# Kernel optimization log

Hardware: AMD Instinct MI355X
Metric: run time of the kernel (lower is better)

Reference implementation:

```python
import jax, jax.numpy as jnp
import numpy as np
from jax import lax

D_H = 1024
RES_DIMS = (512, 256)
LAYERS = 2
T = 8192
ALPHA = 0.1  # reservoir leak rate


def setup_inputs() -> dict:
    key = jax.random.key(0)
    ks = jax.random.split(key, 8)
    s_h = 1.0 / np.sqrt(D_H)
    s_r1 = 1.0 / np.sqrt(RES_DIMS[0])
    s_r2 = 1.0 / np.sqrt(RES_DIMS[1])
    return {
        "x_seq": jax.random.normal(ks[0], (T, D_H), jnp.float32),
        "Wx": jax.random.normal(ks[1], (LAYERS, D_H, D_H), jnp.float32) * s_h,
        "Wh": jax.random.normal(ks[2], (LAYERS, D_H, D_H), jnp.float32) * s_h,
        "b": jnp.zeros((LAYERS, D_H), jnp.float32),
        "V1": jax.random.normal(ks[3], (LAYERS, D_H, RES_DIMS[0]), jnp.float32) * s_r1,
        "U1": jax.random.normal(ks[4], (LAYERS, RES_DIMS[0], D_H), jnp.float32) * s_h,
        "V2": jax.random.normal(ks[5], (LAYERS, D_H, RES_DIMS[1]), jnp.float32) * s_r2,
        "U2": jax.random.normal(ks[6], (LAYERS, RES_DIMS[1], D_H), jnp.float32) * s_h,
    }


def reference(x_seq, Wx, Wh, b, V1, U1, V2, U2):
    # CRSDBlock: stacked recurrent layers, each a time scan with hidden h and
    # two leaky reservoirs. h' = tanh(Wx x + Wh h + V1 r1 + V2 r2 + b);
    # r_i' = (1-a) r_i + a tanh(U_i h').
    d_h = Wx.shape[-1]
    d_r1, d_r2 = U1.shape[1], U2.shape[1]
    dt = x_seq.dtype
    for l in range(Wx.shape[0]):
        wx, wh, bb = Wx[l], Wh[l], b[l]
        v1, u1, v2, u2 = V1[l], U1[l], V2[l], U2[l]

        def step(carry, x_t):
            h, r1, r2 = carry
            h = jnp.tanh(x_t @ wx.T + h @ wh.T + r1 @ v1.T + r2 @ v2.T + bb)
            r1 = (1.0 - ALPHA) * r1 + ALPHA * jnp.tanh(h @ u1.T)
            r2 = (1.0 - ALPHA) * r2 + ALPHA * jnp.tanh(h @ u2.T)
            return (h, r1, r2), h

        init = (jnp.zeros((d_h,), dt), jnp.zeros((d_r1,), dt), jnp.zeros((d_r2,), dt))
        _, x_seq = lax.scan(step, init, x_seq)
    return x_seq
```

## Files before the change

### kernel.cpp

```cpp
#include <hip/hip_runtime.h>

#define D_HH   1024
#define DR1    512
#define DR2    256
#define RTOT   (DR1 + DR2)
#define TSTEPS 8192

#define NB     64
#define BS     512
#define HA     (D_HH / NB)
#define QA     (RTOT / NB)
#define NROWB  (HA + QA)
#define RING   64
#define RMASK  (RING - 1)
#define NREP   4

typedef __attribute__((ext_vector_type(2))) unsigned long long ull2;

__device__ __forceinline__ float dot4f(float4 a, float4 b) {
    return fmaf(a.x, b.x, fmaf(a.y, b.y, fmaf(a.z, b.z, a.w * b.w)));
}

__device__ __forceinline__ ull2 ld16(const unsigned long long* p) {
    ull2 v;
    asm volatile("global_load_dwordx4 %0, %1, off sc0 sc1\n\ts_waitcnt vmcnt(0)"
                 : "=&v"(v) : "v"(p) : "memory");
    return v;
}
__device__ __forceinline__ void ld16x2(const unsigned long long* p0,
                                       const unsigned long long* p1,
                                       ull2& a, ull2& b) {
    asm volatile("global_load_dwordx4 %0, %2, off sc0 sc1\n\t"
                 "global_load_dwordx4 %1, %3, off sc0 sc1\n\t"
                 "s_waitcnt vmcnt(0)"
                 : "=&v"(a), "=&v"(b) : "v"(p0), "v"(p1) : "memory");
}
__device__ __forceinline__ unsigned long long ld8(const unsigned long long* p) {
    unsigned long long v;
    asm volatile("global_load_dwordx2 %0, %1, off sc0 sc1\n\ts_waitcnt vmcnt(0)"
                 : "=&v"(v) : "v"(p) : "memory");
    return v;
}
__device__ __forceinline__ void st16(unsigned long long* p,
                                     unsigned long long lo, unsigned long long hi) {
    ull2 pv; pv[0] = lo; pv[1] = hi;
    asm volatile("global_store_dwordx4 %0, %1, off sc0 sc1"
                 :: "v"(p), "v"(pv) : "memory");
}
__device__ __forceinline__ void st8(unsigned long long* p, int tag, unsigned pay) {
    unsigned long long pv = ((unsigned long long)(unsigned)tag << 32) | pay;
    asm volatile("global_store_dwordx2 %0, %1, off sc0 sc1"
                 :: "v"(p), "v"(pv) : "memory");
}
__device__ __forceinline__ unsigned long long mktag(int tag, float v) {
    return ((unsigned long long)(unsigned)tag << 32) | __float_as_uint(v);
}

__global__ __launch_bounds__(BS, 2) void crsd_fused(
    const float* __restrict__ x,
    const float* __restrict__ Wx,
    const float* __restrict__ Wh,
    const float* __restrict__ bias,
    const float* __restrict__ V1,
    const float* __restrict__ U1,
    const float* __restrict__ V2,
    const float* __restrict__ U2,
    float* __restrict__ out,
    unsigned long long* ring,
    unsigned long long* h1rep,
    unsigned long long* h2rep,
    unsigned long long* r1rep,
    unsigned long long* r2rep,
    unsigned long long* prog)
{
    const int gid = blockIdx.x;
    const int lay = gid >> 6;
    const int g   = gid & (NB - 1);
    const int tid = threadIdx.x;

    const float* wxp = Wx + (size_t)lay * D_HH * D_HH;
    const float* whp = Wh + (size_t)lay * D_HH * D_HH;
    const float* v1p = V1 + (size_t)lay * D_HH * DR1;
    const float* v2p = V2 + (size_t)lay * D_HH * DR2;
    const float* u1p = U1 + (size_t)lay * DR1 * D_HH;
    const float* u2p = U2 + (size_t)lay * DR2 * D_HH;
    const float* bp  = bias + (size_t)lay * D_HH;
    unsigned long long* rrep = lay ? r2rep : r1rep;
    unsigned long long* hrep = lay ? h2rep : h1rep;
    const int rep = g & (NREP - 1);

    __shared__ __align__(16) float r_s[RTOT];
    __shared__ __align__(16) float h_s[D_HH];
    __shared__ __align__(16) float x_s[D_HH];
    __shared__ float zw[HA];

    const int rA = tid >> 5;
    const int p  = tid & 31;
    const int iA = g * HA + rA;
    float4 wa[6];
    {
        const float4* v1r = (const float4*)(v1p + (size_t)iA * DR1);
#pragma unroll
        for (int k = 0; k < 4; ++k) wa[k] = v1r[p + 32 * k];
        const float4* v2r = (const float4*)(v2p + (size_t)iA * DR2);
#pragma unroll
        for (int k = 0; k < 2; ++k) wa[4 + k] = v2r[p + 32 * k];
    }

    const int rB = tid >> 4;
    const int q  = tid & 15;
    const bool isZ = (rB < HA);
    const bool isQ = (rB >= HA) && (rB < NROWB);
    int jG = 0;
    float bi = 0.f;
    const float* brow = whp;
    const float* xrow = whp;
    if (isZ) {
        brow = whp + (size_t)(g * HA + rB) * D_HH;
        xrow = wxp + (size_t)(g * HA + rB) * D_HH;
        bi   = bp[g * HA + rB];
    } else if (isQ) {
        jG = g * QA + (rB - HA);
        brow = (jG < DR1) ? (u1p + (size_t)jG * D_HH)
                          : (u2p + (size_t)(jG - DR1) * D_HH);
    }
    float4 wb[16], wxr[16];
    {
        const float4* br = (const float4*)brow;
        const float4* xr = (const float4*)xrow;
#pragma unroll
        for (int k = 0; k < 16; ++k) { wb[k] = br[q + 16 * k]; wxr[k] = xr[q + 16 * k]; }
    }

    float rloc0 = 0.f, rloc1 = 0.f;
    int   l2c   = 0;

    if (lay == 0) {
        float2 xv = *(const float2*)&x[2 * tid];
        *(float2*)&x_s[2 * tid] = xv;
    } else {
        const unsigned long long* px0 = &ring[2 * tid];
        for (;;) {
            ull2 v = ld16(px0);
            if ((int)(v[0] >> 32) >= 1 && (int)(v[1] >> 32) >= 1) {
                *(float2*)&x_s[2 * tid] =
                    make_float2(__uint_as_float((unsigned)v[0]),
                                __uint_as_float((unsigned)v[1]));
                break;
            }
            __builtin_amdgcn_s_sleep(1);
        }
    }
    __syncthreads();
    if (isZ) {
        const float4* x4 = (const float4*)x_s;
        float acc = 0.f;
#pragma unroll
        for (int k = 0; k < 16; ++k) acc += dot4f(wxr[k], x4[q + 16 * k]);
#pragma unroll
        for (int m = 8; m >= 1; m >>= 1) acc += __shfl_xor(acc, m);
        if (q == 0) zw[rB] = bi + acc;
    }

    for (int t = 0; t < TSTEPS; ++t) {
        if (lay == 0 && tid == 0 && t - 60 > l2c) {
            for (;;) {
                unsigned long long v = ld8(prog);
                if ((int)(v >> 32) >= t - 60) { l2c = (int)(v >> 32); break; }
                __builtin_amdgcn_s_sleep(1);
            }
        }

        if (tid < RTOT / 2) {
            const unsigned long long* pr = &rrep[rep * RTOT + 2 * tid];
            for (;;) {
                ull2 v = ld16(pr);
                if ((int)(v[0] >> 32) >= t && (int)(v[1] >> 32) >= t) {
                    *(float2*)&r_s[2 * tid] =
                        make_float2(__uint_as_float((unsigned)v[0]),
                                    __uint_as_float((unsigned)v[1]));
                    break;
                }
                __builtin_amdgcn_s_sleep(1);
            }
        }
        __syncthreads();

        {
            const float4* r1v = (const float4*)r_s;
            const float4* r2v = (const float4*)(r_s + DR1);
            float acc = dot4f(wa[0], r1v[p]);
            acc += dot4f(wa[1], r1v[p + 32]);
            acc += dot4f(wa[2], r1v[p + 64]);
            acc += dot4f(wa[3], r1v[p + 96]);
            acc += dot4f(wa[4], r2v[p]);
            acc += dot4f(wa[5], r2v[p + 32]);
#pragma unroll
            for (int m = 16; m >= 1; m >>= 1) acc += __shfl_xor(acc, m);
            float hv  = tanhf(zw[rA] + acc);
            float hvp = __shfl_xor(hv, 32);
            if ((tid & 63) == 0) {
                unsigned long long e0 = mktag(t + 1, hv);
                unsigned long long e1 = mktag(t + 1, hvp);
#pragma unroll
                for (int k = 0; k < NREP; ++k)
                    st16(&hrep[k * D_HH + iA], e0, e1);
                if (lay == 0) {
                    st16(&ring[(size_t)(t & RMASK) * D_HH + iA], e0, e1);
                } else {
                    *(float2*)&out[(size_t)t * D_HH + iA] = make_float2(hv, hvp);
                    if (iA == 0) st8(prog, t + 1, 0u);
                }
                *(float2*)&h_s[iA] = make_float2(hv, hvp);
            }
        }

        if (lay == 0) {
            const int ti = (t + 1 < TSTEPS) ? t + 1 : TSTEPS - 1;
            float2 xv = *(const float2*)&x[(size_t)ti * D_HH + 2 * tid];
            *(float2*)&x_s[2 * tid] = xv;
        }

        {
            bool dh = ((tid >> 3) == g);
            const unsigned long long* ph = &hrep[rep * D_HH + 2 * tid];
            if (lay == 0) {
                if (!dh) {
                    for (;;) {
                        ull2 v = ld16(ph);
                        if ((int)(v[0] >> 32) >= t + 1 && (int)(v[1] >> 32) >= t + 1) {
                            *(float2*)&h_s[2 * tid] =
                                make_float2(__uint_as_float((unsigned)v[0]),
                                            __uint_as_float((unsigned)v[1]));
                            break;
                        }
                        __builtin_amdgcn_s_sleep(1);
                    }
                }
            } else {
                const bool needx = (t + 1 < TSTEPS);
                bool dx = !needx;
                const unsigned long long* px =
                    &ring[(size_t)((t + 1) & RMASK) * D_HH + 2 * tid];
                while (!(dh && dx)) {
                    ull2 a, b;
                    ld16x2(ph, px, a, b);
                    if (!dh && (int)(a[0] >> 32) >= t + 1 && (int)(a[1] >> 32) >= t + 1) {
                        *(float2*)&h_s[2 * tid] =
                            make_float2(__uint_as_float((unsigned)a[0]),
                                        __uint_as_float((unsigned)a[1]));
                        dh = true;
                    }
                    if (!dx && (int)(b[0] >> 32) >= t + 2 && (int)(b[1] >> 32) >= t + 2) {
                        *(float2*)&x_s[2 * tid] =
                            make_float2(__uint_as_float((unsigned)b[0]),
                                        __uint_as_float((unsigned)b[1]));
                        dx = true;
                    }
                    if (!(dh && dx)) __builtin_amdgcn_s_sleep(1);
                }
            }
        }
        __syncthreads();

        if (rB < NROWB) {
            const float4* h4 = (const float4*)h_s;
            float acc = 0.f;
#pragma unroll
            for (int k = 0; k < 16; ++k) acc += dot4f(wb[k], h4[q + 16 * k]);
            if (isZ) {
                const float4* x4 = (const float4*)x_s;
#pragma unroll
                for (int k = 0; k < 16; ++k) acc += dot4f(wxr[k], x4[q + 16 * k]);
            }
#pragma unroll
            for (int m = 8; m >= 1; m >>= 1) acc += __shfl_xor(acc, m);
            if (isZ) {
                if (q == 0) zw[rB] = bi + acc;
            } else {
                float accp = __shfl_xor(acc, 16);
                if (q == 0 && !(rB & 1)) {
                    rloc0 = 0.9f * rloc0 + 0.1f * tanhf(acc);
                    rloc1 = 0.9f * rloc1 + 0.1f * tanhf(accp);
                    unsigned long long e0 = mktag(t + 1, rloc0);
                    unsigned long long e1 = mktag(t + 1, rloc1);
#pragma unroll
                    for (int k = 0; k < NREP; ++k)
                        st16(&rrep[k * RTOT + jG], e0, e1);
                }
            }
        }
    }
}

extern "C" void kernel_launch(void* const* d_in, const int* in_sizes, int n_in,
                              void* d_out, int out_size, void* d_ws, size_t ws_size,
                              hipStream_t stream)
{
    const float* x  = (const float*)d_in[0];
    const float* Wx = (const float*)d_in[1];
    const float* Wh = (const float*)d_in[2];
    const float* b  = (const float*)d_in[3];
    const float* V1 = (const float*)d_in[4];
    const float* U1 = (const float*)d_in[5];
    const float* V2 = (const float*)d_in[6];
    const float* U2 = (const float*)d_in[7];
    float* out = (float*)d_out;

    unsigned long long* ring  = (unsigned long long*)d_ws;
    unsigned long long* h1rep = ring + (size_t)RING * D_HH;
    unsigned long long* h2rep = h1rep + NREP * D_HH;
    unsigned long long* r1rep = h2rep + NREP * D_HH;
    unsigned long long* r2rep = r1rep + NREP * RTOT;
    unsigned long long* prog  = r2rep + NREP * RTOT;
    const size_t stateB =
        ((size_t)RING * D_HH + 2 * NREP * D_HH + 2 * NREP * RTOT + 8) *
        sizeof(unsigned long long);

    hipMemsetAsync(d_ws, 0, stateB, stream);
    crsd_fused<<<dim3(2 * NB), dim3(BS), 0, stream>>>(
        x, Wx, Wh, b, V1, U1, V2, U2, out,
        ring, h1rep, h2rep, r1rep, r2rep, prog);
}
```

Measured before the change: 33.74 ms.

## Halve block count to 32 per layer with 1024 threads and drop state replicas

Repartitions the persistent recurrent kernel from 64 blocks of 512 threads per layer to 32 blocks of 1024 threads, so each block owns twice as many hidden rows and fewer blocks take part in the per-step global handshake. The four-way replication of the h and r state buffers is removed, so each value is published with a single tagged 8-byte store instead of several 16-byte stores. The aim is to cut inter-block synchronisation and store traffic per timestep. In exchange, all pollers now read one shared copy, which may add contention, and each block does more work per step with lower occupancy.

Measured after the change: 60.06 ms. 78.0% more time.

```diff
diff --git a/kernel.cpp b/kernel.cpp
--- a/kernel.cpp
+++ b/kernel.cpp
@@ -6,14 +6,13 @@
 #define RTOT   (DR1 + DR2)
 #define TSTEPS 8192
 
-#define NB     64
-#define BS     512
+#define NB     32
+#define BS     1024
 #define HA     (D_HH / NB)
 #define QA     (RTOT / NB)
 #define NROWB  (HA + QA)
 #define RING   64
 #define RMASK  (RING - 1)
-#define NREP   4
 
 typedef __attribute__((ext_vector_type(2))) unsigned long long ull2;
 
@@ -41,22 +40,13 @@
                  : "=&v"(v) : "v"(p) : "memory");
     return v;
 }
-__device__ __forceinline__ void st16(unsigned long long* p,
-                                     unsigned long long lo, unsigned long long hi) {
-    ull2 pv; pv[0] = lo; pv[1] = hi;
-    asm volatile("global_store_dwordx4 %0, %1, off sc0 sc1"
-                 :: "v"(p), "v"(pv) : "memory");
-}
 __device__ __forceinline__ void st8(unsigned long long* p, int tag, unsigned pay) {
     unsigned long long pv = ((unsigned long long)(unsigned)tag << 32) | pay;
     asm volatile("global_store_dwordx2 %0, %1, off sc0 sc1"
                  :: "v"(p), "v"(pv) : "memory");
 }
-__device__ __forceinline__ unsigned long long mktag(int tag, float v) {
-    return ((unsigned long long)(unsigned)tag << 32) | __float_as_uint(v);
-}
-
-__global__ __launch_bounds__(BS, 2) void crsd_fused(
+
+__global__ __launch_bounds__(BS) void crsd_fused(
     const float* __restrict__ x,
     const float* __restrict__ Wx,
     const float* __restrict__ Wh,
@@ -67,14 +57,14 @@
     const float* __restrict__ U2,
     float* __restrict__ out,
     unsigned long long* ring,
-    unsigned long long* h1rep,
-    unsigned long long* h2rep,
-    unsigned long long* r1rep,
-    unsigned long long* r2rep,
+    unsigned long long* h1s,
+    unsigned long long* h2s,
+    unsigned long long* r1s,
+    unsigned long long* r2s,
     unsigned long long* prog)
 {
     const int gid = blockIdx.x;
-    const int lay = gid >> 6;
+    const int lay = gid >> 5;
     const int g   = gid & (NB - 1);
     const int tid = threadIdx.x;
 
@@ -85,9 +75,8 @@
     const float* u1p = U1 + (size_t)lay * DR1 * D_HH;
     const float* u2p = U2 + (size_t)lay * DR2 * D_HH;
     const float* bp  = bias + (size_t)lay * D_HH;
-    unsigned long long* rrep = lay ? r2rep : r1rep;
-    unsigned long long* hrep = lay ? h2rep : h1rep;
-    const int rep = g & (NREP - 1);
+    unsigned long long* rst  = lay ? r2s : r1s;
+    unsigned long long* hloc = lay ? h2s : h1s;
 
     __shared__ __align__(16) float r_s[RTOT];
     __shared__ __align__(16) float h_s[D_HH];
@@ -132,13 +121,12 @@
         for (int k = 0; k < 16; ++k) { wb[k] = br[q + 16 * k]; wxr[k] = xr[q + 16 * k]; }
     }
 
-    float rloc0 = 0.f, rloc1 = 0.f;
-    int   l2c   = 0;
+    float rloc = 0.f;
+    int   l2c  = 0;
 
     if (lay == 0) {
-        float2 xv = *(const float2*)&x[2 * tid];
-        *(float2*)&x_s[2 * tid] = xv;
-    } else {
+        x_s[tid] = x[tid];
+    } else if (tid < D_HH / 2) {
         const unsigned long long* px0 = &ring[2 * tid];
         for (;;) {
             ull2 v = ld16(px0);
@@ -172,7 +160,7 @@
         }
 
         if (tid < RTOT / 2) {
-            const unsigned long long* pr = &rrep[rep * RTOT + 2 * tid];
+            const unsigned long long* pr = &rst[2 * tid];
             for (;;) {
                 ull2 v = ld16(pr);
                 if ((int)(v[0] >> 32) >= t && (int)(v[1] >> 32) >= t) {
@@ -197,33 +185,28 @@
             acc += dot4f(wa[5], r2v[p + 32]);
 #pragma unroll
             for (int m = 16; m >= 1; m >>= 1) acc += __shfl_xor(acc, m);
-            float hv  = tanhf(zw[rA] + acc);
-            float hvp = __shfl_xor(hv, 32);
-            if ((tid & 63) == 0) {
-                unsigned long long e0 = mktag(t + 1, hv);
-                unsigned long long e1 = mktag(t + 1, hvp);
-#pragma unroll
-                for (int k = 0; k < NREP; ++k)
-                    st16(&hrep[k * D_HH + iA], e0, e1);
+            if (p == 0) {
+                float hv = tanhf(zw[rA] + acc);
+                unsigned hb = __float_as_uint(hv);
+                st8(&hloc[iA], t + 1, hb);
                 if (lay == 0) {
-                    st16(&ring[(size_t)(t & RMASK) * D_HH + iA], e0, e1);
+                    st8(&ring[(size_t)(t & RMASK) * D_HH + iA], t + 1, hb);
                 } else {
-                    *(float2*)&out[(size_t)t * D_HH + iA] = make_float2(hv, hvp);
+                    out[(size_t)t * D_HH + iA] = hv;
                     if (iA == 0) st8(prog, t + 1, 0u);
                 }
-                *(float2*)&h_s[iA] = make_float2(hv, hvp);
+                h_s[iA] = hv;
             }
         }
 
         if (lay == 0) {
             const int ti = (t + 1 < TSTEPS) ? t + 1 : TSTEPS - 1;
-            float2 xv = *(const float2*)&x[(size_t)ti * D_HH + 2 * tid];
-            *(float2*)&x_s[2 * tid] = xv;
-        }
-
-        {
-            bool dh = ((tid >> 3) == g);
-            const unsigned long long* ph = &hrep[rep * D_HH + 2 * tid];
+            x_s[tid] = x[(size_t)ti * D_HH + tid];
+        }
+
+        if (tid < D_HH / 2) {
+            bool dh = ((tid >> 4) == g);
+            const unsigned long long* ph = &hloc[2 * tid];
             if (lay == 0) {
                 if (!dh) {
                     for (;;) {
@@ -275,18 +258,12 @@
             }
 #pragma unroll
             for (int m = 8; m >= 1; m >>= 1) acc += __shfl_xor(acc, m);
-            if (isZ) {
-                if (q == 0) zw[rB] = bi + acc;
-            } else {
-                float accp = __shfl_xor(acc, 16);
-                if (q == 0 && !(rB & 1)) {
-                    rloc0 = 0.9f * rloc0 + 0.1f * tanhf(acc);
-                    rloc1 = 0.9f * rloc1 + 0.1f * tanhf(accp);
-                    unsigned long long e0 = mktag(t + 1, rloc0);
-                    unsigned long long e1 = mktag(t + 1, rloc1);
-#pragma unroll
-                    for (int k = 0; k < NREP; ++k)
-                        st16(&rrep[k * RTOT + jG], e0, e1);
+            if (q == 0) {
+                if (isZ) {
+                    zw[rB] = bi + acc;
+                } else {
+                    rloc = 0.9f * rloc + 0.1f * tanhf(acc);
+                    st8(&rst[jG], t + 1, __float_as_uint(rloc));
                 }
             }
         }
@@ -307,18 +284,17 @@
     const float* U2 = (const float*)d_in[7];
     float* out = (float*)d_out;
 
-    unsigned long long* ring  = (unsigned long long*)d_ws;
-    unsigned long long* h1rep = ring + (size_t)RING * D_HH;
-    unsigned long long* h2rep = h1rep + NREP * D_HH;
-    unsigned long long* r1rep = h2rep + NREP * D_HH;
-    unsigned long long* r2rep = r1rep + NREP * RTOT;
-    unsigned long long* prog  = r2rep + NREP * RTOT;
+    unsigned long long* ring = (unsigned long long*)d_ws;
+    unsigned long long* h1s  = ring + (size_t)RING * D_HH;
+    unsigned long long* h2s  = h1s + D_HH;
+    unsigned long long* r1s  = h2s + D_HH;
+    unsigned long long* r2s  = r1s + RTOT;
+    unsigned long long* prog = r2s + RTOT;
     const size_t stateB =
-        ((size_t)RING * D_HH + 2 * NREP * D_HH + 2 * NREP * RTOT + 8) *
-        sizeof(unsigned long long);
+        ((size_t)RING * D_HH + 2 * D_HH + 2 * RTOT + 8) * sizeof(unsigned long long);
 
     hipMemsetAsync(d_ws, 0, stateB, stream);
     crsd_fused<<<dim3(2 * NB), dim3(BS), 0, stream>>>(
         x, Wx, Wh, b, V1, U1, V2, U2, out,
-        ring, h1rep, h2rep, r1rep, r2rep, prog);
-}
+        ring, h1s, h2s, r1s, r2s, prog);
+}
```
